# Performance work log

Hardware: AMD Instinct MI355X
Metric: run time of the kernel (lower is better)

The kernel has to match this reference:

```python
import jax, jax.numpy as jnp
import numpy as np

LOG2_HASHMAP_SIZE = 19
HASHMAP_MASK = np.uint32((1 << LOG2_HASHMAP_SIZE) - 1)
# num_mf_layers=4 -> mf_layer_indices=[2,5,8,11] of the 12-level geometric
# resolution list between base=16 and finest=512
RESOLUTIONS = (30, 80, 210, 512)
PRIMES = (np.uint32(1), np.uint32(11614769), np.uint32(2654435761))
N_POINTS = 2_000_000
N_FEATS = 2

# 8 corner offsets of a 3D voxel, shape [8, 3]
CORNER_OFFSETS = jnp.array([[i, j, k] for i in (0, 1) for j in (0, 1) for k in (0, 1)], dtype=jnp.int32)


def _hash3(coords):
    # coords: [..., 3] int32 grid coordinates -> [...] int32 hash index
    c = coords.astype(jnp.uint32)
    h = (c[..., 0] * PRIMES[0]) ^ (c[..., 1] * PRIMES[1]) ^ (c[..., 2] * PRIMES[2])
    return (h & HASHMAP_MASK).astype(jnp.int32)


def setup_inputs() -> dict:
    key = jax.random.key(0)
    k1, k2 = jax.random.split(key)
    # points inside the unit bounding box
    x = jax.random.uniform(k1, (N_POINTS, 3), dtype=jnp.float32)
    # 4 hash tables, init U(-1e-4, 1e-4) as in nn.init.uniform_
    tables = jax.random.uniform(k2, (len(RESOLUTIONS), 1 << LOG2_HASHMAP_SIZE, N_FEATS),
                                minval=-1e-4, maxval=1e-4, dtype=jnp.float32)
    return {"x": x, "tables": tables}


def reference(x, tables):
    # x: [N, 3] in [0, 1]; tables: [L, 2^19, F]
    outs = []
    for li, res in enumerate(RESOLUTIONS):
        scaled = x * jnp.float32(res)          # [N, 3]
        bottom = jnp.floor(scaled)             # voxel min vertex
        t = scaled - bottom                    # relative position in voxel, [N, 3]
        corners = bottom.astype(jnp.int32)[:, None, :] + CORNER_OFFSETS[None]  # [N, 8, 3]
        idx = _hash3(corners)                  # [N, 8]
        emb = tables[li][idx]                  # gather corner embeddings, [N, 8, F]
        # trilinear weights: prod over dims of (t if offset==1 else 1-t)
        w = jnp.where(CORNER_OFFSETS[None].astype(bool), t[:, None, :], 1.0 - t[:, None, :]).prod(axis=-1)  # [N, 8]
        outs.append(jnp.einsum('nc,ncf->nf', w, emb))  # [N, F]
    return jnp.concatenate(outs, axis=-1)  # [N, L*F] = [N, 8]
```

## Files before the change

kernel.cpp:

```cpp
#include <hip/hip_runtime.h>
#include <stdint.h>

#define LOG2_HASHMAP_SIZE 19
#define HASHMAP_SIZE (1u << LOG2_HASHMAP_SIZE)
#define HASHMAP_MASK (HASHMAP_SIZE - 1u)
#define N_LEVELS 4

__device__ __forceinline__ float2 level_embed_p(float px, float py, float pz,
                                                const float* __restrict__ tables,
                                                int li, float r)
{
    const uint32_t P1 = 11614769u;
    const uint32_t P2 = 2654435761u;

    const float sx = px * r, sy = py * r, sz = pz * r;
    const float bx = floorf(sx), by = floorf(sy), bz = floorf(sz);
    const float tx = sx - bx, ty = sy - by, tz = sz - bz;
    const float ux = 1.0f - tx, uy = 1.0f - ty, uz = 1.0f - tz;

    const uint32_t ix = (uint32_t)(int)bx;
    const uint32_t iy = (uint32_t)(int)by;
    const uint32_t iz = (uint32_t)(int)bz;

    const uint32_t hy0 = iy * P1, hy1 = (iy + 1u) * P1;
    const uint32_t hz0 = iz * P2, hz1 = (iz + 1u) * P2;

    uint32_t S[4];
    float W[4];
    S[0] = hy0 ^ hz0;  W[0] = uy * uz;
    S[1] = hy0 ^ hz1;  W[1] = uy * tz;
    S[2] = hy1 ^ hz0;  W[2] = ty * uz;
    S[3] = hy1 ^ hz1;  W[3] = ty * tz;

    const float* tab = tables + (size_t)li * HASHMAP_SIZE * 2;
    const float2* __restrict__ tab2 = (const float2*)tab;
    const float4* __restrict__ tab4 = (const float4*)tab;

    float f0 = 0.0f, f1 = 0.0f;

    if ((ix & 1u) == 0u) {
        #pragma unroll
        for (int c = 0; c < 4; ++c) {
            const uint32_t h0 = (ix ^ S[c]) & HASHMAP_MASK;
            const float4 v = tab4[h0 >> 1];
            const bool hi = (h0 & 1u);
            const float e0x = hi ? v.z : v.x;
            const float e0y = hi ? v.w : v.y;
            const float e1x = hi ? v.x : v.z;
            const float e1y = hi ? v.y : v.w;
            f0 += W[c] * (ux * e0x + tx * e1x);
            f1 += W[c] * (ux * e0y + tx * e1y);
        }
    } else {
        #pragma unroll
        for (int c = 0; c < 4; ++c) {
            const uint32_t h0 = (ix ^ S[c]) & HASHMAP_MASK;
            const uint32_t h1 = ((ix + 1u) ^ S[c]) & HASHMAP_MASK;
            const float2 e0 = tab2[h0];
            const float2 e1 = tab2[h1];
            f0 += W[c] * (ux * e0.x + tx * e1.x);
            f1 += W[c] * (ux * e0.y + tx * e1.y);
        }
    }
    return make_float2(f0, f1);
}

__global__ __launch_bounds__(256) void pass_ws_kernel(
    const float* __restrict__ x, const float* __restrict__ tables,
    float2* __restrict__ ws, int li, float r, int n)
{
    const int i = blockIdx.x * blockDim.x + threadIdx.x;
    if (i >= n) return;
    const float px = x[3 * (size_t)i + 0];
    const float py = x[3 * (size_t)i + 1];
    const float pz = x[3 * (size_t)i + 2];
    ws[i] = level_embed_p(px, py, pz, tables, li, r);
}

__global__ __launch_bounds__(256) void final_kernel(
    const float* __restrict__ x, const float* __restrict__ tables,
    const float2* __restrict__ ws0, const float2* __restrict__ ws1,
    const float2* __restrict__ ws2, float* __restrict__ out, int n)
{
    const int i = blockIdx.x * blockDim.x + threadIdx.x;
    if (i >= n) return;
    const float px = x[3 * (size_t)i + 0];
    const float py = x[3 * (size_t)i + 1];
    const float pz = x[3 * (size_t)i + 2];
    const float2 e3 = level_embed_p(px, py, pz, tables, 3, 512.0f);
    const float2 e0 = ws0[i];
    const float2 e1 = ws1[i];
    const float2 e2 = ws2[i];
    float4* op = (float4*)(out + 8 * (size_t)i);
    op[0] = make_float4(e0.x, e0.y, e1.x, e1.y);
    op[1] = make_float4(e2.x, e2.y, e3.x, e3.y);
}

__global__ __launch_bounds__(256) void pass_direct_kernel(
    const float* __restrict__ x, const float* __restrict__ tables,
    float* __restrict__ out, int li, float r, int n)
{
    const int i = blockIdx.x * blockDim.x + threadIdx.x;
    if (i >= n) return;
    const float px = x[3 * (size_t)i + 0];
    const float py = x[3 * (size_t)i + 1];
    const float pz = x[3 * (size_t)i + 2];
    const float2 e = level_embed_p(px, py, pz, tables, li, r);
    float2* op = (float2*)(out + 8 * (size_t)i + 2 * li);
    *op = e;
}

extern "C" void kernel_launch(void* const* d_in, const int* in_sizes, int n_in,
                              void* d_out, int out_size, void* d_ws, size_t ws_size,
                              hipStream_t stream) {
    const float* x = (const float*)d_in[0];
    const float* tables = (const float*)d_in[1];
    float* out = (float*)d_out;
    const int n = in_sizes[0] / 3;

    const float res[N_LEVELS] = {30.0f, 80.0f, 210.0f, 512.0f};
    const int block = 256;
    const int grid = (n + block - 1) / block;

    const size_t ws_needed = 3 * (size_t)n * sizeof(float2);
    if (ws_size >= ws_needed) {
        float2* ws = (float2*)d_ws;
        for (int li = 0; li < 3; ++li) {
            pass_ws_kernel<<<grid, block, 0, stream>>>(
                x, tables, ws + (size_t)li * n, li, res[li], n);
        }
        final_kernel<<<grid, block, 0, stream>>>(
            x, tables, ws, ws + (size_t)n, ws + 2 * (size_t)n, out, n);
    } else {
        for (int li = 0; li < N_LEVELS; ++li) {
            pass_direct_kernel<<<grid, block, 0, stream>>>(
                x, tables, out, li, res[li], n);
        }
    }
}
```

Measured before the change: 282.5 us.

## Process two points per thread and split gathers into issue and resolve phases

Each thread in the workspace and final kernels now handles two points. All hash-table gathers for both points are issued before any interpolation runs, which raises memory-level parallelism per thread. The trilinear math moves into a separate resolve step that works on a fragment of loaded float4s with precomputed select weights, and point coordinates are read as float2 vectors. In exchange the kernels use more registers and launch half as many threads, which can lower occupancy on a latency-bound gather workload.

```diff
diff --git a/kernel.cpp b/kernel.cpp
--- a/kernel.cpp
+++ b/kernel.cpp
@@ -6,9 +6,16 @@
 #define HASHMAP_MASK (HASHMAP_SIZE - 1u)
 #define N_LEVELS 4
 
-__device__ __forceinline__ float2 level_embed_p(float px, float py, float pz,
-                                                const float* __restrict__ tables,
-                                                int li, float r)
+struct LevelFrag {
+    float4 v[4];
+    float  W[4];
+    float  wl[4];
+    float  wh[4];
+};
+
+__device__ __forceinline__ void level_issue(
+    float px, float py, float pz,
+    const float* __restrict__ tables, int li, float r, LevelFrag& F)
 {
     const uint32_t P1 = 11614769u;
     const uint32_t P2 = 2654435761u;
@@ -26,41 +33,44 @@
     const uint32_t hz0 = iz * P2, hz1 = (iz + 1u) * P2;
 
     uint32_t S[4];
-    float W[4];
-    S[0] = hy0 ^ hz0;  W[0] = uy * uz;
-    S[1] = hy0 ^ hz1;  W[1] = uy * tz;
-    S[2] = hy1 ^ hz0;  W[2] = ty * uz;
-    S[3] = hy1 ^ hz1;  W[3] = ty * tz;
+    S[0] = hy0 ^ hz0;  F.W[0] = uy * uz;
+    S[1] = hy0 ^ hz1;  F.W[1] = uy * tz;
+    S[2] = hy1 ^ hz0;  F.W[2] = ty * uz;
+    S[3] = hy1 ^ hz1;  F.W[3] = ty * tz;
 
     const float* tab = tables + (size_t)li * HASHMAP_SIZE * 2;
     const float2* __restrict__ tab2 = (const float2*)tab;
     const float4* __restrict__ tab4 = (const float4*)tab;
-
-    float f0 = 0.0f, f1 = 0.0f;
 
     if ((ix & 1u) == 0u) {
         #pragma unroll
         for (int c = 0; c < 4; ++c) {
             const uint32_t h0 = (ix ^ S[c]) & HASHMAP_MASK;
-            const float4 v = tab4[h0 >> 1];
-            const bool hi = (h0 & 1u);
-            const float e0x = hi ? v.z : v.x;
-            const float e0y = hi ? v.w : v.y;
-            const float e1x = hi ? v.x : v.z;
-            const float e1y = hi ? v.y : v.w;
-            f0 += W[c] * (ux * e0x + tx * e1x);
-            f1 += W[c] * (ux * e0y + tx * e1y);
+            F.v[c] = tab4[h0 >> 1];
+            const bool hi = (S[c] & 1u) != 0u;
+            F.wl[c] = hi ? tx : ux;
+            F.wh[c] = hi ? ux : tx;
         }
     } else {
         #pragma unroll
         for (int c = 0; c < 4; ++c) {
             const uint32_t h0 = (ix ^ S[c]) & HASHMAP_MASK;
             const uint32_t h1 = ((ix + 1u) ^ S[c]) & HASHMAP_MASK;
-            const float2 e0 = tab2[h0];
-            const float2 e1 = tab2[h1];
-            f0 += W[c] * (ux * e0.x + tx * e1.x);
-            f1 += W[c] * (ux * e0.y + tx * e1.y);
-        }
+            ((float2*)&F.v[c])[0] = tab2[h0];
+            ((float2*)&F.v[c])[1] = tab2[h1];
+            F.wl[c] = ux;
+            F.wh[c] = tx;
+        }
+    }
+}
+
+__device__ __forceinline__ float2 level_resolve(const LevelFrag& F)
+{
+    float f0 = 0.0f, f1 = 0.0f;
+    #pragma unroll
+    for (int c = 0; c < 4; ++c) {
+        f0 += F.W[c] * (F.wl[c] * F.v[c].x + F.wh[c] * F.v[c].z);
+        f1 += F.W[c] * (F.wl[c] * F.v[c].y + F.wh[c] * F.v[c].w);
     }
     return make_float2(f0, f1);
 }
@@ -68,44 +78,98 @@
 __global__ __launch_bounds__(256) void pass_ws_kernel(
     const float* __restrict__ x, const float* __restrict__ tables,
     float2* __restrict__ ws, int li, float r, int n)
+{
+    const int t = blockIdx.x * blockDim.x + threadIdx.x;
+    const int i0 = 2 * t;
+    if (i0 >= n) return;
+    const bool two = (i0 + 1 < n);
+
+    float pxA, pyA, pzA, pxB, pyB, pzB;
+    if (two) {
+        const float2* __restrict__ x2 = (const float2*)x;
+        const float2 q0 = x2[3 * (size_t)t + 0];
+        const float2 q1 = x2[3 * (size_t)t + 1];
+        const float2 q2 = x2[3 * (size_t)t + 2];
+        pxA = q0.x; pyA = q0.y; pzA = q1.x;
+        pxB = q1.y; pyB = q2.x; pzB = q2.y;
+    } else {
+        pxA = x[3 * (size_t)i0 + 0];
+        pyA = x[3 * (size_t)i0 + 1];
+        pzA = x[3 * (size_t)i0 + 2];
+        pxB = pxA; pyB = pyA; pzB = pzA;
+    }
+
+    LevelFrag FA, FB;
+    level_issue(pxA, pyA, pzA, tables, li, r, FA);
+    level_issue(pxB, pyB, pzB, tables, li, r, FB);
+    const float2 rA = level_resolve(FA);
+    const float2 rB = level_resolve(FB);
+    ws[i0] = rA;
+    if (two) ws[i0 + 1] = rB;
+}
+
+__global__ __launch_bounds__(256) void final_kernel(
+    const float* __restrict__ x, const float* __restrict__ tables,
+    const float2* __restrict__ ws0, const float2* __restrict__ ws1,
+    const float2* __restrict__ ws2, float* __restrict__ out, int n)
+{
+    const int t = blockIdx.x * blockDim.x + threadIdx.x;
+    const int i0 = 2 * t;
+    if (i0 >= n) return;
+    const bool two = (i0 + 1 < n);
+
+    float pxA, pyA, pzA, pxB, pyB, pzB;
+    if (two) {
+        const float2* __restrict__ x2 = (const float2*)x;
+        const float2 q0 = x2[3 * (size_t)t + 0];
+        const float2 q1 = x2[3 * (size_t)t + 1];
+        const float2 q2 = x2[3 * (size_t)t + 2];
+        pxA = q0.x; pyA = q0.y; pzA = q1.x;
+        pxB = q1.y; pyB = q2.x; pzB = q2.y;
+    } else {
+        pxA = x[3 * (size_t)i0 + 0];
+        pyA = x[3 * (size_t)i0 + 1];
+        pzA = x[3 * (size_t)i0 + 2];
+        pxB = pxA; pyB = pyA; pzB = pzA;
+    }
+
+    LevelFrag FA, FB;
+    level_issue(pxA, pyA, pzA, tables, 3, 512.0f, FA);
+    level_issue(pxB, pyB, pzB, tables, 3, 512.0f, FB);
+
+    const float2 a0 = ws0[i0];
+    const float2 a1 = ws1[i0];
+    const float2 a2 = ws2[i0];
+    const int iB = two ? (i0 + 1) : i0;
+    const float2 b0 = ws0[iB];
+    const float2 b1 = ws1[iB];
+    const float2 b2 = ws2[iB];
+
+    const float2 a3 = level_resolve(FA);
+    const float2 b3 = level_resolve(FB);
+
+    float4* opA = (float4*)(out + 8 * (size_t)i0);
+    opA[0] = make_float4(a0.x, a0.y, a1.x, a1.y);
+    opA[1] = make_float4(a2.x, a2.y, a3.x, a3.y);
+    if (two) {
+        float4* opB = (float4*)(out + 8 * (size_t)(i0 + 1));
+        opB[0] = make_float4(b0.x, b0.y, b1.x, b1.y);
+        opB[1] = make_float4(b2.x, b2.y, b3.x, b3.y);
+    }
+}
+
+__global__ __launch_bounds__(256) void pass_direct_kernel(
+    const float* __restrict__ x, const float* __restrict__ tables,
+    float* __restrict__ out, int li, float r, int n)
 {
     const int i = blockIdx.x * blockDim.x + threadIdx.x;
     if (i >= n) return;
     const float px = x[3 * (size_t)i + 0];
     const float py = x[3 * (size_t)i + 1];
     const float pz = x[3 * (size_t)i + 2];
-    ws[i] = level_embed_p(px, py, pz, tables, li, r);
-}
-
-__global__ __launch_bounds__(256) void final_kernel(
-    const float* __restrict__ x, const float* __restrict__ tables,
-    const float2* __restrict__ ws0, const float2* __restrict__ ws1,
-    const float2* __restrict__ ws2, float* __restrict__ out, int n)
-{
-    const int i = blockIdx.x * blockDim.x + threadIdx.x;
-    if (i >= n) return;
-    const float px = x[3 * (size_t)i + 0];
-    const float py = x[3 * (size_t)i + 1];
-    const float pz = x[3 * (size_t)i + 2];
-    const float2 e3 = level_embed_p(px, py, pz, tables, 3, 512.0f);
-    const float2 e0 = ws0[i];
-    const float2 e1 = ws1[i];
-    const float2 e2 = ws2[i];
-    float4* op = (float4*)(out + 8 * (size_t)i);
-    op[0] = make_float4(e0.x, e0.y, e1.x, e1.y);
-    op[1] = make_float4(e2.x, e2.y, e3.x, e3.y);
-}
-
-__global__ __launch_bounds__(256) void pass_direct_kernel(
-    const float* __restrict__ x, const float* __restrict__ tables,
-    float* __restrict__ out, int li, float r, int n)
-{
-    const int i = blockIdx.x * blockDim.x + threadIdx.x;
-    if (i >= n) return;
-    const float px = x[3 * (size_t)i + 0];
-    const float py = x[3 * (size_t)i + 1];
-    const float pz = x[3 * (size_t)i + 2];
-    const float2 e = level_embed_p(px, py, pz, tables, li, r);
+    LevelFrag F;
+    level_issue(px, py, pz, tables, li, r, F);
+    const float2 e = level_resolve(F);
     float2* op = (float2*)(out + 8 * (size_t)i + 2 * li);
     *op = e;
 }
@@ -120,18 +184,19 @@
 
     const float res[N_LEVELS] = {30.0f, 80.0f, 210.0f, 512.0f};
     const int block = 256;
-    const int grid = (n + block - 1) / block;
+    const int grid2 = ((n + 1) / 2 + block - 1) / block;
 
     const size_t ws_needed = 3 * (size_t)n * sizeof(float2);
     if (ws_size >= ws_needed) {
         float2* ws = (float2*)d_ws;
         for (int li = 0; li < 3; ++li) {
-            pass_ws_kernel<<<grid, block, 0, stream>>>(
+            pass_ws_kernel<<<grid2, block, 0, stream>>>(
                 x, tables, ws + (size_t)li * n, li, res[li], n);
         }
-        final_kernel<<<grid, block, 0, stream>>>(
+        final_kernel<<<grid2, block, 0, stream>>>(
             x, tables, ws, ws + (size_t)n, ws + 2 * (size_t)n, out, n);
     } else {
+        const int grid = (n + block - 1) / block;
         for (int li = 0; li < N_LEVELS; ++li) {
             pass_direct_kernel<<<grid, block, 0, stream>>>(
                 x, tables, out, li, res[li], n);
```

New measurement: 360.0 us. 27.5% more time.
